# Kernel optimization log

Hardware: AMD Instinct MI355X
Metric: run time of the kernel (lower is better)

The kernel has to match this reference:

```python
import jax, jax.numpy as jnp
import numpy as np

# Static problem dims (match input_specs / init_kwargs)
B, NF, H, W = 4, 8, 512, 512
C = 8  # number of instance labels; all assumed present -> torch.unique == arange(C)
DELTA_V, DELTA_D = 0.5, 1.5
ALPHA, BETA, GAMMA = 1.0, 1.0, 0.001


def _safe_norm_from_sq(sq):
    # sqrt with zero-safe gradient (double-where trick)
    pos = sq > 0
    return jnp.where(pos, jnp.sqrt(jnp.where(pos, sq, 1.0)), 0.0)


def setup_inputs() -> dict:
    key = jax.random.key(0)
    k1, k2 = jax.random.split(key)
    prediction = jax.random.normal(k1, (B, NF, H, W), dtype=jnp.float32)
    target = jax.random.randint(k2, (B, H, W), 0, C).astype(jnp.int32)
    return {"prediction": prediction, "target": target}


def _per_sample_loss(pred, tgt):
    # pred: (NF, H, W) float, tgt: (H, W) int labels in [0, C)
    N = H * W
    p = pred.reshape(NF, N)                      # (NF, N)
    g = tgt.reshape(N)                           # (N,)
    onehot = (g[:, None] == jnp.arange(C)[None, :]).astype(p.dtype)  # (N, C)
    counts = onehot.sum(axis=0)                  # (C,) pixels per instance

    # per-instance means: sum(pred * mask) / count  -> (NF, C)
    sums = jnp.einsum('fn,nc->fc', p, onehot)
    means = sums / counts

    # l_var (faithful to original quirk: distance summed over ALL pixels &
    # clusters, then divided by each per-cluster count and summed):
    # diff = || (mu - pred) * mask || over feature dim
    diffvec = (means[:, None, :] - p[:, :, None]) * onehot[None, :, :]  # (NF, N, C)
    diff = _safe_norm_from_sq(jnp.sum(diffvec * diffvec, axis=0))       # (N, C)
    distance = jnp.clip(diff - DELTA_V, 0.0, 100000.0) ** 2
    l_var = (distance.sum() / counts).sum() / C

    # l_dist: pairwise inter-cluster margin
    m = means.T                                   # (C, NF)
    pd = m[:, None, :] - m[None, :, :]            # (C, C, NF)
    norm = _safe_norm_from_sq(jnp.sum(pd * pd, axis=2))  # (C, C)
    margin = 2.0 * DELTA_D * (1.0 - jnp.eye(C, dtype=p.dtype))
    l_dist = jnp.sum(jnp.clip(margin - norm, 0.0, 100000.0) ** 2) / (C * (C - 1))

    # l_reg
    l_reg = (_safe_norm_from_sq(jnp.sum(means * means, axis=0)) / C).sum()

    return ALPHA * l_var + BETA * l_dist + GAMMA * l_reg


def reference(prediction, target):
    losses = jax.vmap(_per_sample_loss)(prediction, target)  # (B,)
    return losses.sum() / B
```

## Files before the change

kernel.cpp:

```cpp
#include <hip/hip_runtime.h>

#define N_PIX (512*512)
#define NFEAT 8
#define NCLUS 8
#define NB    4
#define GRIDX 128
#define NCHUNK (N_PIX/4)
#define STRIDE (GRIDX*256)
#define PART_TOTAL (72*NB*GRIDX)
#define DIST_OFF  PART_TOTAL
#define S2_OFF    (DIST_OFF + NB*GRIDX)

__global__ __launch_bounds__(256) void k_sums(const float* __restrict__ pred,
                                              const int* __restrict__ tgt,
                                              float* __restrict__ ws) {
    const int tid = threadIdx.x;
    const int bx = blockIdx.x, b = blockIdx.y;
    const int lane = tid & 63, w = tid >> 6;

    float acc[64];
#pragma unroll
    for (int i = 0; i < 64; ++i) acc[i] = 0.0f;
    int cnt[8] = {0, 0, 0, 0, 0, 0, 0, 0};

    const int4*   t4 = (const int4*)(tgt + b * N_PIX);
    const float4* p4 = (const float4*)(pred + (size_t)b * NFEAT * N_PIX);

#pragma unroll
    for (int it = 0; it < NCHUNK / STRIDE; ++it) {
        const int i = bx * 256 + tid + it * STRIDE;
        int4 g4 = t4[i];
        int gs[4] = {g4.x, g4.y, g4.z, g4.w};
        float pr[NFEAT][4];
#pragma unroll
        for (int f = 0; f < NFEAT; ++f) {
            float4 v = p4[f * NCHUNK + i];
            pr[f][0] = v.x; pr[f][1] = v.y; pr[f][2] = v.z; pr[f][3] = v.w;
        }
#pragma unroll
        for (int j = 0; j < 4; ++j) {
            float m[NCLUS];
#pragma unroll
            for (int c = 0; c < NCLUS; ++c) {
                bool hit = (gs[j] == c);
                m[c] = hit ? 1.0f : 0.0f;
                cnt[c] += (int)__popcll(__ballot(hit));
            }
#pragma unroll
            for (int f = 0; f < NFEAT; ++f)
#pragma unroll
                for (int c = 0; c < NCLUS; ++c)
                    acc[f * 8 + c] = fmaf(m[c], pr[f][j], acc[f * 8 + c]);
        }
    }

#pragma unroll
    for (int k = 0; k < 6; ++k) {
        const int d = 1 << k;
        const int bit = (lane >> k) & 1;
#pragma unroll
        for (int p = 0; p < (64 >> 1); ++p) {
            if (p >= (64 >> (k + 1))) break;
            float a  = __shfl_xor(acc[2 * p],     d, 64);
            float bb = __shfl_xor(acc[2 * p + 1], d, 64);
            float own = bit ? acc[2 * p + 1] : acc[2 * p];
            float oth = bit ? bb : a;
            acc[p] = own + oth;
        }
    }

    __shared__ float ssum[4][64];
    __shared__ float scnt[4][8];
    ssum[w][lane] = acc[0];
    if (lane == 0) {
#pragma unroll
        for (int c = 0; c < NCLUS; ++c) scnt[w][c] = (float)cnt[c];
    }
    __syncthreads();

    if (tid < 72) {
        float s;
        if (tid < 64) s = ssum[0][tid] + ssum[1][tid] + ssum[2][tid] + ssum[3][tid];
        else { int c = tid - 64; s = scnt[0][c] + scnt[1][c] + scnt[2][c] + scnt[3][c]; }
        ws[tid * (NB * GRIDX) + b * GRIDX + bx] = s;
    }
}

__global__ __launch_bounds__(256) void k_var(const float* __restrict__ pred,
                                             const int* __restrict__ tgt,
                                             float* __restrict__ ws) {
    __shared__ float pp[72][4];
    __shared__ float raw[72];
    __shared__ float mean[NCLUS * 9];
    __shared__ float sl[4];
    const int tid = threadIdx.x;
    const int bx = blockIdx.x, b = blockIdx.y;

    for (int s = tid; s < 288; s += 256) {
        const int e = s >> 2, q = s & 3;
        const float4* src = (const float4*)(ws + e * (NB * GRIDX) + b * GRIDX) + q * 8;
        float4 a0 = src[0], a1 = src[1], a2 = src[2], a3 = src[3];
        float4 a4 = src[4], a5 = src[5], a6 = src[6], a7 = src[7];
        float r0 = (a0.x + a0.y + a0.z + a0.w) + (a1.x + a1.y + a1.z + a1.w);
        float r1 = (a2.x + a2.y + a2.z + a2.w) + (a3.x + a3.y + a3.z + a3.w);
        float r2 = (a4.x + a4.y + a4.z + a4.w) + (a5.x + a5.y + a5.z + a5.w);
        float r3 = (a6.x + a6.y + a6.z + a6.w) + (a7.x + a7.y + a7.z + a7.w);
        pp[e][q] = (r0 + r1) + (r2 + r3);
    }
    __syncthreads();
    if (tid < 72) {
        float s = (pp[tid][0] + pp[tid][1]) + (pp[tid][2] + pp[tid][3]);
        raw[tid] = s;
        if (bx == 0) ws[S2_OFF + b * 72 + tid] = s;
    }
    __syncthreads();
    if (tid < 64) {
        const int f = tid >> 3, c = tid & 7;
        mean[c * 9 + f] = raw[f * 8 + c] / raw[64 + c];
    }
    __syncthreads();

    const int4*   t4 = (const int4*)(tgt + b * N_PIX);
    const float4* p4 = (const float4*)(pred + (size_t)b * NFEAT * N_PIX);

    float local = 0.0f;
#pragma unroll
    for (int it = 0; it < NCHUNK / STRIDE; ++it) {
        const int i = bx * 256 + tid + it * STRIDE;
        int4 g4 = t4[i];
        int gs[4] = {g4.x, g4.y, g4.z, g4.w};
        float pr[NFEAT][4];
#pragma unroll
        for (int f = 0; f < NFEAT; ++f) {
            float4 v = p4[f * NCHUNK + i];
            pr[f][0] = v.x; pr[f][1] = v.y; pr[f][2] = v.z; pr[f][3] = v.w;
        }
#pragma unroll
        for (int j = 0; j < 4; ++j) {
            const float* m = &mean[gs[j] * 9];
            float dsq = 0.0f;
#pragma unroll
            for (int f = 0; f < NFEAT; ++f) {
                float d = m[f] - pr[f][j];
                dsq = fmaf(d, d, dsq);
            }
            float diff = sqrtf(dsq);
            float dm = fminf(fmaxf(diff - 0.5f, 0.0f), 100000.0f);
            local = fmaf(dm, dm, local);
        }
    }

#pragma unroll
    for (int o = 32; o >= 1; o >>= 1) local += __shfl_xor(local, o, 64);
    if ((tid & 63) == 0) sl[tid >> 6] = local;
    __syncthreads();
    if (tid == 0)
        ws[DIST_OFF + bx * NB + b] = sl[0] + sl[1] + sl[2] + sl[3];
}

__global__ __launch_bounds__(256) void k_final(const float* __restrict__ ws,
                                               float* __restrict__ out) {
    __shared__ float sd[256];
    __shared__ float meanL[NB][64];
    __shared__ float sl[NB];
    const int tid = threadIdx.x;

    sd[tid] = ws[DIST_OFF + tid] + ws[DIST_OFF + 256 + tid];
    __syncthreads();
#pragma unroll
    for (int off = 128; off >= 4; off >>= 1) {
        if (tid < off) sd[tid] += sd[tid + off];
        __syncthreads();
    }

    const int b = tid >> 6, idx = tid & 63;
    const float* S2 = ws + S2_OFF + b * 72;
    meanL[b][idx] = S2[idx] / S2[64 + (idx & 7)];
    __syncthreads();

    const int i = idx >> 3, j = idx & 7;
    float pdsq = 0.0f;
#pragma unroll
    for (int f = 0; f < 8; ++f) {
        float d = meanL[b][f * 8 + i] - meanL[b][f * 8 + j];
        pdsq = fmaf(d, d, pdsq);
    }
    float nrm = sqrtf(pdsq);
    float t = fminf(fmaxf(3.0f - nrm, 0.0f), 100000.0f);
    float val = (i == j) ? 0.0f : t * t * (1.0f / 56.0f);

    if (i == 0) {
        float rsq = 0.0f;
#pragma unroll
        for (int f = 0; f < 8; ++f) {
            float m = meanL[b][f * 8 + j];
            rsq = fmaf(m, m, rsq);
        }
        float invc = 1.0f / S2[64 + j];
        val += 0.001f * sqrtf(rsq) * 0.125f + sd[b] * invc * 0.125f;
    }

#pragma unroll
    for (int o = 32; o >= 1; o >>= 1) val += __shfl_xor(val, o, 64);
    if (idx == 0) sl[b] = val;
    __syncthreads();
    if (tid == 0) out[0] = (sl[0] + sl[1] + sl[2] + sl[3]) * 0.25f;
}

extern "C" void kernel_launch(void* const* d_in, const int* in_sizes, int n_in,
                              void* d_out, int out_size, void* d_ws, size_t ws_size,
                              hipStream_t stream) {
    const float* pred = (const float*)d_in[0];
    const int*   tgt  = (const int*)d_in[1];
    float* out = (float*)d_out;
    float* ws  = (float*)d_ws;

    dim3 grid(GRIDX, NB);
    k_sums<<<grid, 256, 0, stream>>>(pred, tgt, ws);
    k_var <<<grid, 256, 0, stream>>>(pred, tgt, ws);
    k_final<<<1, 256, 0, stream>>>(ws, out);
}
```

Measured before the change: 88.25 us.

## Fuse three kernels into one persistent kernel with grid barriers and register reuse

```diff
diff --git a/kernel.cpp b/kernel.cpp
--- a/kernel.cpp
+++ b/kernel.cpp
@@ -5,44 +5,80 @@
 #define NCLUS 8
 #define NB    4
 #define GRIDX 128
+#define NBLOCKS (GRIDX*NB)
 #define NCHUNK (N_PIX/4)
 #define STRIDE (GRIDX*256)
+#define NITER  (NCHUNK/STRIDE)
 #define PART_TOTAL (72*NB*GRIDX)
 #define DIST_OFF  PART_TOTAL
 #define S2_OFF    (DIST_OFF + NB*GRIDX)
-
-__global__ __launch_bounds__(256) void k_sums(const float* __restrict__ pred,
-                                              const int* __restrict__ tgt,
-                                              float* __restrict__ ws) {
+#define CTR_OFF   (S2_OFF + NB*72)
+
+__device__ __forceinline__ void grid_barrier(unsigned* ctr) {
+    __syncthreads();
+    if (threadIdx.x == 0) {
+        __threadfence();
+        __hip_atomic_fetch_add(ctr, 1u, __ATOMIC_RELAXED, __HIP_MEMORY_SCOPE_AGENT);
+        int guard = 0;
+        while (__hip_atomic_load(ctr, __ATOMIC_RELAXED, __HIP_MEMORY_SCOPE_AGENT)
+               < (unsigned)NBLOCKS) {
+            if (++guard > (1 << 24)) break;
+        }
+        __threadfence();
+    }
+    __syncthreads();
+}
+
+__global__ __launch_bounds__(256, 2) void k_fused(const float* __restrict__ pred,
+                                                  const int* __restrict__ tgt,
+                                                  float* __restrict__ ws,
+                                                  float* __restrict__ out) {
+    __shared__ float ssum[4][64];
+    __shared__ float scnt[4][8];
+    __shared__ float pp[72][4];
+    __shared__ float raw[72];
+    __shared__ float mean[NCLUS * 9];
+    __shared__ float slv[4];
+    __shared__ float sd[256];
+    __shared__ float meanL[NB][64];
+    __shared__ float slf[NB];
+
     const int tid = threadIdx.x;
     const int bx = blockIdx.x, b = blockIdx.y;
     const int lane = tid & 63, w = tid >> 6;
+    unsigned* ctr = (unsigned*)(ws + CTR_OFF);
+
+    const int4*   t4 = (const int4*)(tgt + b * N_PIX);
+    const float4* p4 = (const float4*)(pred + (size_t)b * NFEAT * N_PIX);
+
+    int   gss[NITER][4];
+    float prs[NITER][NFEAT][4];
+#pragma unroll
+    for (int it = 0; it < NITER; ++it) {
+        const int i = bx * 256 + tid + it * STRIDE;
+        int4 g4 = t4[i];
+        gss[it][0] = g4.x; gss[it][1] = g4.y; gss[it][2] = g4.z; gss[it][3] = g4.w;
+#pragma unroll
+        for (int f = 0; f < NFEAT; ++f) {
+            float4 v = p4[f * NCHUNK + i];
+            prs[it][f][0] = v.x; prs[it][f][1] = v.y;
+            prs[it][f][2] = v.z; prs[it][f][3] = v.w;
+        }
+    }
 
     float acc[64];
 #pragma unroll
     for (int i = 0; i < 64; ++i) acc[i] = 0.0f;
     int cnt[8] = {0, 0, 0, 0, 0, 0, 0, 0};
 
-    const int4*   t4 = (const int4*)(tgt + b * N_PIX);
-    const float4* p4 = (const float4*)(pred + (size_t)b * NFEAT * N_PIX);
-
-#pragma unroll
-    for (int it = 0; it < NCHUNK / STRIDE; ++it) {
-        const int i = bx * 256 + tid + it * STRIDE;
-        int4 g4 = t4[i];
-        int gs[4] = {g4.x, g4.y, g4.z, g4.w};
-        float pr[NFEAT][4];
-#pragma unroll
-        for (int f = 0; f < NFEAT; ++f) {
-            float4 v = p4[f * NCHUNK + i];
-            pr[f][0] = v.x; pr[f][1] = v.y; pr[f][2] = v.z; pr[f][3] = v.w;
-        }
+#pragma unroll
+    for (int it = 0; it < NITER; ++it) {
 #pragma unroll
         for (int j = 0; j < 4; ++j) {
             float m[NCLUS];
 #pragma unroll
             for (int c = 0; c < NCLUS; ++c) {
-                bool hit = (gs[j] == c);
+                bool hit = (gss[it][j] == c);
                 m[c] = hit ? 1.0f : 0.0f;
                 cnt[c] += (int)__popcll(__ballot(hit));
             }
@@ -50,7 +86,7 @@
             for (int f = 0; f < NFEAT; ++f)
 #pragma unroll
                 for (int c = 0; c < NCLUS; ++c)
-                    acc[f * 8 + c] = fmaf(m[c], pr[f][j], acc[f * 8 + c]);
+                    acc[f * 8 + c] = fmaf(m[c], prs[it][f][j], acc[f * 8 + c]);
         }
     }
 
@@ -62,39 +98,27 @@
         for (int p = 0; p < (64 >> 1); ++p) {
             if (p >= (64 >> (k + 1))) break;
             float a  = __shfl_xor(acc[2 * p],     d, 64);
-            float bb = __shfl_xor(acc[2 * p + 1], d, 64);
+            float vb = __shfl_xor(acc[2 * p + 1], d, 64);
             float own = bit ? acc[2 * p + 1] : acc[2 * p];
-            float oth = bit ? bb : a;
+            float oth = bit ? vb : a;
             acc[p] = own + oth;
         }
     }
 
-    __shared__ float ssum[4][64];
-    __shared__ float scnt[4][8];
     ssum[w][lane] = acc[0];
     if (lane == 0) {
 #pragma unroll
         for (int c = 0; c < NCLUS; ++c) scnt[w][c] = (float)cnt[c];
     }
     __syncthreads();
-
     if (tid < 72) {
         float s;
         if (tid < 64) s = ssum[0][tid] + ssum[1][tid] + ssum[2][tid] + ssum[3][tid];
-        else { int c = tid - 64; s = scnt[0][c] + scnt[1][c] + scnt[2][c] + scnt[3][c]; }
+        else { int c2 = tid - 64; s = scnt[0][c2] + scnt[1][c2] + scnt[2][c2] + scnt[3][c2]; }
         ws[tid * (NB * GRIDX) + b * GRIDX + bx] = s;
     }
-}
-
-__global__ __launch_bounds__(256) void k_var(const float* __restrict__ pred,
-                                             const int* __restrict__ tgt,
-                                             float* __restrict__ ws) {
-    __shared__ float pp[72][4];
-    __shared__ float raw[72];
-    __shared__ float mean[NCLUS * 9];
-    __shared__ float sl[4];
-    const int tid = threadIdx.x;
-    const int bx = blockIdx.x, b = blockIdx.y;
+
+    grid_barrier(ctr + 0);
 
     for (int s = tid; s < 288; s += 256) {
         const int e = s >> 2, q = s & 3;
@@ -120,28 +144,16 @@
     }
     __syncthreads();
 
-    const int4*   t4 = (const int4*)(tgt + b * N_PIX);
-    const float4* p4 = (const float4*)(pred + (size_t)b * NFEAT * N_PIX);
-
     float local = 0.0f;
 #pragma unroll
-    for (int it = 0; it < NCHUNK / STRIDE; ++it) {
-        const int i = bx * 256 + tid + it * STRIDE;
-        int4 g4 = t4[i];
-        int gs[4] = {g4.x, g4.y, g4.z, g4.w};
-        float pr[NFEAT][4];
-#pragma unroll
-        for (int f = 0; f < NFEAT; ++f) {
-            float4 v = p4[f * NCHUNK + i];
-            pr[f][0] = v.x; pr[f][1] = v.y; pr[f][2] = v.z; pr[f][3] = v.w;
-        }
+    for (int it = 0; it < NITER; ++it) {
 #pragma unroll
         for (int j = 0; j < 4; ++j) {
-            const float* m = &mean[gs[j] * 9];
+            const float* mm = &mean[gss[it][j] * 9];
             float dsq = 0.0f;
 #pragma unroll
             for (int f = 0; f < NFEAT; ++f) {
-                float d = m[f] - pr[f][j];
+                float d = mm[f] - prs[it][f][j];
                 dsq = fmaf(d, d, dsq);
             }
             float diff = sqrtf(dsq);
@@ -152,18 +164,14 @@
 
 #pragma unroll
     for (int o = 32; o >= 1; o >>= 1) local += __shfl_xor(local, o, 64);
-    if ((tid & 63) == 0) sl[tid >> 6] = local;
+    if ((tid & 63) == 0) slv[tid >> 6] = local;
     __syncthreads();
     if (tid == 0)
-        ws[DIST_OFF + bx * NB + b] = sl[0] + sl[1] + sl[2] + sl[3];
-}
-
-__global__ __launch_bounds__(256) void k_final(const float* __restrict__ ws,
-                                               float* __restrict__ out) {
-    __shared__ float sd[256];
-    __shared__ float meanL[NB][64];
-    __shared__ float sl[NB];
-    const int tid = threadIdx.x;
+        ws[DIST_OFF + bx * NB + b] = slv[0] + slv[1] + slv[2] + slv[3];
+
+    grid_barrier(ctr + 1);
+
+    if (bx != 0 || b != 0) return;
 
     sd[tid] = ws[DIST_OFF + tid] + ws[DIST_OFF + 256 + tid];
     __syncthreads();
@@ -173,38 +181,38 @@
         __syncthreads();
     }
 
-    const int b = tid >> 6, idx = tid & 63;
-    const float* S2 = ws + S2_OFF + b * 72;
-    meanL[b][idx] = S2[idx] / S2[64 + (idx & 7)];
-    __syncthreads();
-
-    const int i = idx >> 3, j = idx & 7;
+    const int bb = tid >> 6, idx = tid & 63;
+    const float* S2 = ws + S2_OFF + bb * 72;
+    meanL[bb][idx] = S2[idx] / S2[64 + (idx & 7)];
+    __syncthreads();
+
+    const int ii = idx >> 3, jj = idx & 7;
     float pdsq = 0.0f;
 #pragma unroll
     for (int f = 0; f < 8; ++f) {
-        float d = meanL[b][f * 8 + i] - meanL[b][f * 8 + j];
+        float d = meanL[bb][f * 8 + ii] - meanL[bb][f * 8 + jj];
         pdsq = fmaf(d, d, pdsq);
     }
     float nrm = sqrtf(pdsq);
     float t = fminf(fmaxf(3.0f - nrm, 0.0f), 100000.0f);
-    float val = (i == j) ? 0.0f : t * t * (1.0f / 56.0f);
-
-    if (i == 0) {
+    float val = (ii == jj) ? 0.0f : t * t * (1.0f / 56.0f);
+
+    if (ii == 0) {
         float rsq = 0.0f;
 #pragma unroll
         for (int f = 0; f < 8; ++f) {
-            float m = meanL[b][f * 8 + j];
-            rsq = fmaf(m, m, rsq);
-        }
-        float invc = 1.0f / S2[64 + j];
-        val += 0.001f * sqrtf(rsq) * 0.125f + sd[b] * invc * 0.125f;
+            float m2 = meanL[bb][f * 8 + jj];
+            rsq = fmaf(m2, m2, rsq);
+        }
+        float invc = 1.0f / S2[64 + jj];
+        val += 0.001f * sqrtf(rsq) * 0.125f + sd[bb] * invc * 0.125f;
     }
 
 #pragma unroll
     for (int o = 32; o >= 1; o >>= 1) val += __shfl_xor(val, o, 64);
-    if (idx == 0) sl[b] = val;
-    __syncthreads();
-    if (tid == 0) out[0] = (sl[0] + sl[1] + sl[2] + sl[3]) * 0.25f;
+    if (idx == 0) slf[bb] = val;
+    __syncthreads();
+    if (tid == 0) out[0] = (slf[0] + slf[1] + slf[2] + slf[3]) * 0.25f;
 }
 
 extern "C" void kernel_launch(void* const* d_in, const int* in_sizes, int n_in,
@@ -215,8 +223,8 @@
     float* out = (float*)d_out;
     float* ws  = (float*)d_ws;
 
+    hipMemsetAsync((char*)d_ws + (size_t)CTR_OFF * sizeof(float), 0, 8, stream);
+
     dim3 grid(GRIDX, NB);
-    k_sums<<<grid, 256, 0, stream>>>(pred, tgt, ws);
-    k_var <<<grid, 256, 0, stream>>>(pred, tgt, ws);
-    k_final<<<1, 256, 0, stream>>>(ws, out);
+    k_fused<<<grid, 256, 0, stream>>>(pred, tgt, ws, out);
 }
```

Measured after the change: 153.0 us. +73.4%, slower.
